# Performance work log

Measured on AMD Instinct MI355X. Metric: run time of the kernel, lower is better.

Reference implementation:

```python
import jax, jax.numpy as jnp
import numpy as np

N = 50000   # total nodes
E = 600000  # total edges
D = 128     # feature dim (node_dim == all gcn_dims)
G = 128     # graphs in batch
LN_EPS = 1e-5


def setup_inputs() -> dict:
    key = jax.random.key(0)
    ks = jax.random.split(key, 16)
    inp = {
        "x": jax.random.normal(ks[0], (N, D), dtype=jnp.float32),
        "edge_index": jax.random.randint(ks[1], (2, E), 0, N),
        "batch": jnp.sort(jax.random.randint(ks[2], (N,), 0, G)),
    }
    for l in range(3):
        inp[f"W{l}"] = jax.random.normal(ks[3 + 4 * l], (D, D), dtype=jnp.float32) / np.float32(np.sqrt(D))
        inp[f"b{l}"] = jnp.zeros((D,), jnp.float32)
        inp[f"g{l}"] = jnp.ones((D,), jnp.float32)   # LayerNorm weight
        inp[f"be{l}"] = jnp.zeros((D,), jnp.float32)  # LayerNorm bias
    return inp


def _gcn_norm(edge_index):
    # PyG GCNConv default: add self-loops, symmetric deg^-1/2 normalization.
    loop = jnp.arange(N, dtype=edge_index.dtype)
    src = jnp.concatenate([edge_index[0], loop])
    dst = jnp.concatenate([edge_index[1], loop])
    deg = jax.ops.segment_sum(jnp.ones(src.shape[0], jnp.float32), dst, num_segments=N)
    dinv = jnp.where(deg > 0, jax.lax.rsqrt(deg), 0.0)
    norm = dinv[src] * dinv[dst]  # [E+N]
    return src, dst, norm


def _block(x, src, dst, norm, W, b, g, be):
    # GCNConv: gather-transform-scatter
    h = x @ W                                   # [N, D]
    msg = h[src] * norm[:, None]                # [E+N, D] gather + scale
    out = jax.ops.segment_sum(msg, dst, num_segments=N) + b
    # LayerNorm
    mu = jnp.mean(out, axis=-1, keepdims=True)
    var = jnp.mean((out - mu) ** 2, axis=-1, keepdims=True)
    out = (out - mu) * jax.lax.rsqrt(var + LN_EPS) * g + be
    # residual (Identity since in==out channels) + SiLU
    return jax.nn.silu(out + x)


def reference(x, edge_index, batch, W0, b0, g0, be0, W1, b1, g1, be1, W2, b2, g2, be2):
    src, dst, norm = _gcn_norm(edge_index)
    params = [(W0, b0, g0, be0), (W1, b1, g1, be1), (W2, b2, g2, be2)]
    for (W, b, g, be) in params:
        x = _block(x, src, dst, norm, W, b, g, be)
    # global mean pool over batch ids
    counts = jax.ops.segment_sum(jnp.ones((N,), jnp.float32), batch, num_segments=G)
    sums = jax.ops.segment_sum(x, batch, num_segments=G)
    return sums / jnp.maximum(counts, 1.0)[:, None]
```

## Files before the change

kernel.cpp:

```cpp
#include <hip/hip_runtime.h>
#include <math.h>

#define DD 128

typedef __attribute__((ext_vector_type(8))) short short8;
typedef __attribute__((ext_vector_type(4))) float f32x4;

__device__ __forceinline__ unsigned short f2b(float f) {
    unsigned int x = __float_as_uint(f);
    return (unsigned short)((x + 0x7FFFu + ((x >> 16) & 1u)) >> 16);
}
__device__ __forceinline__ float b2f(unsigned short u) {
    return __uint_as_float(((unsigned int)u) << 16);
}

__global__ __launch_bounds__(256) void k_setup(const int* __restrict__ dst, int* __restrict__ cnt, int E,
                                               const float* __restrict__ W0, const float* __restrict__ W1,
                                               const float* __restrict__ W2, unsigned short* __restrict__ T0,
                                               unsigned short* __restrict__ T1, unsigned short* __restrict__ T2) {
    int bid = blockIdx.x;
    if (bid < 192) {
        int l = bid >> 6;
        const float* W = (l == 0) ? W0 : (l == 1) ? W1 : W2;
        unsigned short* WT = (l == 0) ? T0 : (l == 1) ? T1 : T2;
        int idx = (bid & 63) * 256 + threadIdx.x;
        int k = idx >> 7, c = idx & 127;
        WT[c * DD + k] = f2b(W[idx]);
    } else {
        int e = (bid - 192) * 256 + threadIdx.x;
        if (e < E) atomicAdd(&cnt[dst[e]], 1);
    }
}

__global__ __launch_bounds__(256) void k_scan1(const int* __restrict__ cnt, int* __restrict__ part, int N) {
    __shared__ int lds[256];
    int t = threadIdx.x;
    int i = blockIdx.x * 256 + t;
    lds[t] = (i < N) ? cnt[i] : 0;
    __syncthreads();
#pragma unroll
    for (int off = 128; off > 0; off >>= 1) {
        if (t < off) lds[t] += lds[t + off];
        __syncthreads();
    }
    if (t == 0) part[blockIdx.x] = lds[0];
}

__global__ __launch_bounds__(1024) void k_scan2(int* __restrict__ part, int* __restrict__ rowptr,
                                                int nblk, int N) {
    __shared__ int lds[1024];
    int t = threadIdx.x;
    int v = (t < nblk) ? part[t] : 0;
    lds[t] = v;
    __syncthreads();
    for (int off = 1; off < 1024; off <<= 1) {
        int u = (t >= off) ? lds[t - off] : 0;
        __syncthreads();
        lds[t] += u;
        __syncthreads();
    }
    if (t < nblk) part[t] = lds[t] - v;
    if (t == 1023) rowptr[N] = lds[1023];
}

__global__ __launch_bounds__(256) void k_scan3(const int* __restrict__ cnt, const int* __restrict__ part,
                                               int* __restrict__ rowptr, float* __restrict__ dinv, int N) {
    __shared__ int lds[256];
    int t = threadIdx.x;
    int i = blockIdx.x * 256 + t;
    int v = (i < N) ? cnt[i] : 0;
    lds[t] = v;
    __syncthreads();
    for (int off = 1; off < 256; off <<= 1) {
        int u = (t >= off) ? lds[t - off] : 0;
        __syncthreads();
        lds[t] += u;
        __syncthreads();
    }
    if (i < N) {
        rowptr[i] = part[blockIdx.x] + lds[t] - v;
        dinv[i] = rsqrtf((float)v + 1.0f);
    }
}

__global__ __launch_bounds__(256) void k_fill(const int* __restrict__ src, const int* __restrict__ dst,
                                              const float* __restrict__ dinv, const int* __restrict__ rowptr,
                                              int* __restrict__ cursor, int2* __restrict__ adj, int E) {
    int e = blockIdx.x * 256 + threadIdx.x;
    if (e >= E) return;
    int s = src[e], d = dst[e];
    int pos = atomicAdd(&cursor[d], 1);
    float w = dinv[s] * dinv[d];
    adj[rowptr[d] + pos] = make_int2(s, __float_as_int(w));
}

template <int IN_BF16>
__global__ __launch_bounds__(256) void k_gemm_mfma(const void* __restrict__ Xv,
                                                   const unsigned short* __restrict__ WT,
                                                   unsigned short* __restrict__ H, int N) {
    __shared__ __align__(16) unsigned short sB[DD * DD];
    __shared__ __align__(16) unsigned short sA[DD * DD];
    int tid = threadIdx.x;
    long row0 = (long)blockIdx.x * 128;

#pragma unroll
    for (int i = 0; i < 8; ++i) {
        int q = tid + 256 * i;
        int c = q >> 4, j = q & 15;
        short8 v = *(const short8*)(WT + q * 8);
        int byte = c * 256 + ((j * 16) ^ ((c & 7) << 4));
        *(short8*)((char*)sB + byte) = v;
    }
#pragma unroll
    for (int i = 0; i < 8; ++i) {
        int q = tid + 256 * i;
        int r = q >> 4, j = q & 15;
        short8 v;
        if (IN_BF16) {
#pragma unroll
            for (int z = 0; z < 8; ++z) v[z] = 0;
            if (row0 + r < N) v = *(const short8*)((const unsigned short*)Xv + (row0 + r) * DD + j * 8);
        } else {
            float4 a0 = make_float4(0.f, 0.f, 0.f, 0.f), a1 = a0;
            if (row0 + r < N) {
                const float4* p = (const float4*)((const float*)Xv + (row0 + r) * DD + j * 8);
                a0 = p[0];
                a1 = p[1];
            }
            v[0] = (short)f2b(a0.x); v[1] = (short)f2b(a0.y);
            v[2] = (short)f2b(a0.z); v[3] = (short)f2b(a0.w);
            v[4] = (short)f2b(a1.x); v[5] = (short)f2b(a1.y);
            v[6] = (short)f2b(a1.z); v[7] = (short)f2b(a1.w);
        }
        int byte = r * 256 + ((j * 16) ^ ((r & 7) << 4));
        *(short8*)((char*)sA + byte) = v;
    }
    __syncthreads();

    int w = tid >> 6, l = tid & 63;
    int lr = l & 15, kg = l >> 4;
    int ar0 = w * 32 + lr, ar1 = w * 32 + 16 + lr;
    f32x4 acc0[8] = {}, acc1[8] = {};

#pragma unroll
    for (int step = 0; step < 4; ++step) {
        int koff = step * 64 + kg * 16;
        short8 a0 = *(const short8*)((const char*)sA + ar0 * 256 + (koff ^ ((ar0 & 7) << 4)));
        short8 a1 = *(const short8*)((const char*)sA + ar1 * 256 + (koff ^ ((ar1 & 7) << 4)));
#pragma unroll
        for (int ct = 0; ct < 8; ++ct) {
            int c = ct * 16 + lr;
            short8 bf = *(const short8*)((const char*)sB + c * 256 + (koff ^ ((c & 7) << 4)));
            acc0[ct] = __builtin_amdgcn_mfma_f32_16x16x32_bf16(a0, bf, acc0[ct], 0, 0, 0);
            acc1[ct] = __builtin_amdgcn_mfma_f32_16x16x32_bf16(a1, bf, acc1[ct], 0, 0, 0);
        }
    }

#pragma unroll
    for (int ct = 0; ct < 8; ++ct) {
#pragma unroll
        for (int reg = 0; reg < 4; ++reg) {
            long r = row0 + w * 32 + kg * 4 + reg;
            if (r < N) H[r * DD + ct * 16 + lr] = f2b(acc0[ct][reg]);
            long r2 = r + 16;
            if (r2 < N) H[r2 * DD + ct * 16 + lr] = f2b(acc1[ct][reg]);
        }
    }
}

template <int IN_BF16>
__global__ __launch_bounds__(256) void k_agg(const unsigned short* __restrict__ h, const void* __restrict__ xin,
                                             const int* __restrict__ rowptr, const int2* __restrict__ adj,
                                             const float* __restrict__ dinv, const float* __restrict__ b,
                                             const float* __restrict__ g, const float* __restrict__ be,
                                             unsigned int* __restrict__ xout, int N) {
    int row = blockIdx.x * 4 + (threadIdx.x >> 6);
    if (row >= N) return;
    int lane = threadIdx.x & 63;
    const unsigned int* hu = (const unsigned int*)h;

    float dv = dinv[row];
    float dv2 = dv * dv;
    unsigned int us = hu[(size_t)row * 64 + lane];
    float2 bv = ((const float2*)b)[lane];
    float2 acc = make_float2(fmaf(b2f((unsigned short)(us & 0xFFFF)), dv2, bv.x),
                             fmaf(b2f((unsigned short)(us >> 16)), dv2, bv.y));

    int beg = rowptr[row], end = rowptr[row + 1];
    for (int j0 = beg; j0 < end; j0 += 64) {
        int myj = j0 + lane;
        int2 a = make_int2(0, 0);
        if (myj < end) a = adj[myj];
        int cnt = min(64, end - j0);
        int cntR = (cnt + 15) & ~15;
        for (int k0 = 0; k0 < cntR; k0 += 16) {
            unsigned int un[16];
            float wt[16];
#pragma unroll
            for (int u = 0; u < 16; ++u) {
                int s = __shfl(a.x, k0 + u, 64);
                wt[u] = __int_as_float(__shfl(a.y, k0 + u, 64));
                un[u] = hu[(size_t)s * 64 + lane];
            }
#pragma unroll
            for (int u = 0; u < 16; ++u) {
                acc.x = fmaf(wt[u], b2f((unsigned short)(un[u] & 0xFFFF)), acc.x);
                acc.y = fmaf(wt[u], b2f((unsigned short)(un[u] >> 16)), acc.y);
            }
        }
    }

    float ssum = acc.x + acc.y;
#pragma unroll
    for (int o = 32; o > 0; o >>= 1) ssum += __shfl_xor(ssum, o, 64);
    float mu = ssum * (1.0f / 128.0f);
    float dx0 = acc.x - mu, dx1 = acc.y - mu;
    float vs = dx0 * dx0 + dx1 * dx1;
#pragma unroll
    for (int o = 32; o > 0; o >>= 1) vs += __shfl_xor(vs, o, 64);
    float rstd = rsqrtf(vs * (1.0f / 128.0f) + 1e-5f);

    float2 gv = ((const float2*)g)[lane];
    float2 bev = ((const float2*)be)[lane];
    float2 xv;
    if (IN_BF16) {
        unsigned int xu = ((const unsigned int*)xin)[(size_t)row * 64 + lane];
        xv = make_float2(b2f((unsigned short)(xu & 0xFFFF)), b2f((unsigned short)(xu >> 16)));
    } else {
        xv = ((const float2*)xin)[(size_t)row * 64 + lane];
    }
    float a0 = fmaf(dx0 * rstd, gv.x, bev.x) + xv.x;
    float a1 = fmaf(dx1 * rstd, gv.y, bev.y) + xv.y;
    a0 = a0 / (1.0f + expf(-a0));
    a1 = a1 / (1.0f + expf(-a1));
    xout[(size_t)row * 64 + lane] = ((unsigned int)f2b(a1) << 16) | (unsigned int)f2b(a0);
}

__global__ __launch_bounds__(256) void k_pool2(const unsigned int* __restrict__ x, const int* __restrict__ batch,
                                               float* __restrict__ out, int N) {
    int gi = blockIdx.x;
    int lo = 0, hi = N;
    while (lo < hi) { int m = (lo + hi) >> 1; if (batch[m] < gi) lo = m + 1; else hi = m; }
    int beg = lo;
    lo = beg; hi = N;
    while (lo < hi) { int m = (lo + hi) >> 1; if (batch[m] < gi + 1) lo = m + 1; else hi = m; }
    int end = lo;

    int tid = threadIdx.x;
    int wave = tid >> 6, lane = tid & 63;
    float2 acc = make_float2(0.f, 0.f);
    for (int r = beg + wave; r < end; r += 4) {
        unsigned int u = x[(size_t)r * 64 + lane];
        acc.x += b2f((unsigned short)(u & 0xFFFF));
        acc.y += b2f((unsigned short)(u >> 16));
    }
    __shared__ float part[4][DD];
    ((float2*)part[wave])[lane] = acc;
    __syncthreads();
    if (wave == 0) {
        float sx = 0.f, sy = 0.f;
#pragma unroll
        for (int w = 0; w < 4; ++w) {
            float2 v = ((const float2*)part[w])[lane];
            sx += v.x;
            sy += v.y;
        }
        float inv = 1.0f / fmaxf((float)(end - beg), 1.0f);
        ((float2*)(out + (size_t)gi * DD))[lane] = make_float2(sx * inv, sy * inv);
    }
}

extern "C" void kernel_launch(void* const* d_in, const int* in_sizes, int n_in,
                              void* d_out, int out_size, void* d_ws, size_t ws_size,
                              hipStream_t stream) {
    const float* x = (const float*)d_in[0];
    const int* edge = (const int*)d_in[1];
    const int* batch = (const int*)d_in[2];
    const float* W[3] = {(const float*)d_in[3], (const float*)d_in[7], (const float*)d_in[11]};
    const float* b[3] = {(const float*)d_in[4], (const float*)d_in[8], (const float*)d_in[12]};
    const float* g[3] = {(const float*)d_in[5], (const float*)d_in[9], (const float*)d_in[13]};
    const float* be[3] = {(const float*)d_in[6], (const float*)d_in[10], (const float*)d_in[14]};

    int N = in_sizes[0] / DD;
    int E = in_sizes[1] / 2;
    int G = out_size / DD;
    const int* srcI = edge;
    const int* dstI = edge + E;

    int nblk = (N + 255) / 256;

    char* ws = (char*)d_ws;
    size_t ND = (size_t)N * DD;
    unsigned int* bufX = (unsigned int*)ws;           ws += ND * 2;
    unsigned short* bufH = (unsigned short*)ws;       ws += ND * 2;
    unsigned short* wt[3];
    for (int l = 0; l < 3; ++l) { wt[l] = (unsigned short*)ws; ws += (size_t)DD * DD * 2; }
    float* dinv = (float*)ws;                         ws += (size_t)N * 4;
    int* cnt = (int*)ws;                              ws += (size_t)N * 4;
    int* cursor = (int*)ws;                           ws += (size_t)N * 4;
    int* rowptr = (int*)ws;                           ws += (size_t)(N + 1) * 4;
    int* part = (int*)ws;                             ws += (size_t)nblk * 4;
    ws = (char*)(((uintptr_t)ws + 15) & ~(uintptr_t)15);
    int2* adj = (int2*)ws;

    hipMemsetAsync(cnt, 0, (size_t)N * 2 * 4, stream);

    k_setup<<<192 + (E + 255) / 256, 256, 0, stream>>>(dstI, cnt, E, W[0], W[1], W[2], wt[0], wt[1], wt[2]);
    k_scan1<<<nblk, 256, 0, stream>>>(cnt, part, N);
    k_scan2<<<1, 1024, 0, stream>>>(part, rowptr, nblk, N);
    k_scan3<<<nblk, 256, 0, stream>>>(cnt, part, rowptr, dinv, N);
    k_fill<<<(E + 255) / 256, 256, 0, stream>>>(srcI, dstI, dinv, rowptr, cursor, adj, E);

    int gblk = (N + 127) / 128, ablk = (N + 3) / 4;
    k_gemm_mfma<0><<<gblk, 256, 0, stream>>>(x, wt[0], bufH, N);
    k_agg<0><<<ablk, 256, 0, stream>>>(bufH, x, rowptr, adj, dinv, b[0], g[0], be[0], bufX, N);
    for (int l = 1; l < 3; ++l) {
        k_gemm_mfma<1><<<gblk, 256, 0, stream>>>(bufX, wt[l], bufH, N);
        k_agg<1><<<ablk, 256, 0, stream>>>(bufH, bufX, rowptr, adj, dinv, b[l], g[l], be[l], bufX, N);
    }

    k_pool2<<<G, 256, 0, stream>>>(bufX, batch, (float*)d_out, N);
}
```

Baseline: 238.8 us.

## Fold GCN normalization into GEMM output and bucket CSR build

The source-side deg^-1/2 scale now happens in the GEMM epilogue, and the destination-side scale is applied once after aggregation. This lets the adjacency store only 4-byte source indices instead of (src, weight) pairs, halving index traffic in each of the three aggregation passes. The CSR fill is split into a bucketed binning pass over 32-node buckets plus a per-bucket placement pass that uses LDS atomics, replacing global per-node atomics. The cost is an extra kernel and a temporary edge buffer, and rounding changes slightly because the scale is applied before the bf16 conversion.

```diff
diff --git a/kernel.cpp b/kernel.cpp
--- a/kernel.cpp
+++ b/kernel.cpp
@@ -83,20 +83,38 @@
     }
 }
 
-__global__ __launch_bounds__(256) void k_fill(const int* __restrict__ src, const int* __restrict__ dst,
-                                              const float* __restrict__ dinv, const int* __restrict__ rowptr,
-                                              int* __restrict__ cursor, int2* __restrict__ adj, int E) {
+__global__ __launch_bounds__(256) void k_bin(const int* __restrict__ src, const int* __restrict__ dst,
+                                             const int* __restrict__ rowptr, int* __restrict__ bcur,
+                                             int2* __restrict__ tmp, int E) {
     int e = blockIdx.x * 256 + threadIdx.x;
     if (e >= E) return;
     int s = src[e], d = dst[e];
-    int pos = atomicAdd(&cursor[d], 1);
-    float w = dinv[s] * dinv[d];
-    adj[rowptr[d] + pos] = make_int2(s, __float_as_int(w));
+    int b = d >> 5;
+    int base = rowptr[b << 5];
+    int slot = atomicAdd(&bcur[b], 1);
+    tmp[base + slot] = make_int2(s, d);
+}
+
+__global__ __launch_bounds__(256) void k_place(const int* __restrict__ rowptr, const int2* __restrict__ tmp,
+                                               int* __restrict__ adjS, int N) {
+    int b = blockIdx.x;
+    int d0 = b << 5;
+    int dend = min(d0 + 32, N);
+    int base = rowptr[d0], endp = rowptr[dend];
+    __shared__ int lcur[32];
+    if (threadIdx.x < 32) lcur[threadIdx.x] = 0;
+    __syncthreads();
+    for (int i = base + threadIdx.x; i < endp; i += 256) {
+        int2 sd = tmp[i];
+        int pos = atomicAdd(&lcur[sd.y - d0], 1);
+        adjS[rowptr[sd.y] + pos] = sd.x;
+    }
 }
 
 template <int IN_BF16>
 __global__ __launch_bounds__(256) void k_gemm_mfma(const void* __restrict__ Xv,
                                                    const unsigned short* __restrict__ WT,
+                                                   const float* __restrict__ dinv,
                                                    unsigned short* __restrict__ H, int N) {
     __shared__ __align__(16) unsigned short sB[DD * DD];
     __shared__ __align__(16) unsigned short sA[DD * DD];
@@ -156,21 +174,28 @@
         }
     }
 
+    float dv0[4], dv1[4];
+#pragma unroll
+    for (int reg = 0; reg < 4; ++reg) {
+        long r = row0 + w * 32 + kg * 4 + reg;
+        dv0[reg] = (r < N) ? dinv[r] : 0.f;
+        dv1[reg] = (r + 16 < N) ? dinv[r + 16] : 0.f;
+    }
 #pragma unroll
     for (int ct = 0; ct < 8; ++ct) {
 #pragma unroll
         for (int reg = 0; reg < 4; ++reg) {
             long r = row0 + w * 32 + kg * 4 + reg;
-            if (r < N) H[r * DD + ct * 16 + lr] = f2b(acc0[ct][reg]);
+            if (r < N) H[r * DD + ct * 16 + lr] = f2b(dv0[reg] * acc0[ct][reg]);
             long r2 = r + 16;
-            if (r2 < N) H[r2 * DD + ct * 16 + lr] = f2b(acc1[ct][reg]);
+            if (r2 < N) H[r2 * DD + ct * 16 + lr] = f2b(dv1[reg] * acc1[ct][reg]);
         }
     }
 }
 
 template <int IN_BF16>
 __global__ __launch_bounds__(256) void k_agg(const unsigned short* __restrict__ h, const void* __restrict__ xin,
-                                             const int* __restrict__ rowptr, const int2* __restrict__ adj,
+                                             const int* __restrict__ rowptr, const int* __restrict__ adjS,
                                              const float* __restrict__ dinv, const float* __restrict__ b,
                                              const float* __restrict__ g, const float* __restrict__ be,
                                              unsigned int* __restrict__ xout, int N) {
@@ -180,41 +205,42 @@
     const unsigned int* hu = (const unsigned int*)h;
 
     float dv = dinv[row];
-    float dv2 = dv * dv;
     unsigned int us = hu[(size_t)row * 64 + lane];
-    float2 bv = ((const float2*)b)[lane];
-    float2 acc = make_float2(fmaf(b2f((unsigned short)(us & 0xFFFF)), dv2, bv.x),
-                             fmaf(b2f((unsigned short)(us >> 16)), dv2, bv.y));
+    float selfx = b2f((unsigned short)(us & 0xFFFF));
+    float selfy = b2f((unsigned short)(us >> 16));
+    float2 acc = make_float2(0.f, 0.f);
 
     int beg = rowptr[row], end = rowptr[row + 1];
     for (int j0 = beg; j0 < end; j0 += 64) {
         int myj = j0 + lane;
-        int2 a = make_int2(0, 0);
-        if (myj < end) a = adj[myj];
+        int a = (myj < end) ? adjS[myj] : 0;
         int cnt = min(64, end - j0);
         int cntR = (cnt + 15) & ~15;
         for (int k0 = 0; k0 < cntR; k0 += 16) {
             unsigned int un[16];
-            float wt[16];
 #pragma unroll
             for (int u = 0; u < 16; ++u) {
-                int s = __shfl(a.x, k0 + u, 64);
-                wt[u] = __int_as_float(__shfl(a.y, k0 + u, 64));
+                int s = __shfl(a, k0 + u, 64);
                 un[u] = hu[(size_t)s * 64 + lane];
             }
 #pragma unroll
             for (int u = 0; u < 16; ++u) {
-                acc.x = fmaf(wt[u], b2f((unsigned short)(un[u] & 0xFFFF)), acc.x);
-                acc.y = fmaf(wt[u], b2f((unsigned short)(un[u] >> 16)), acc.y);
+                float m = (k0 + u < cnt) ? 1.0f : 0.0f;
+                acc.x = fmaf(m, b2f((unsigned short)(un[u] & 0xFFFF)), acc.x);
+                acc.y = fmaf(m, b2f((unsigned short)(un[u] >> 16)), acc.y);
             }
         }
     }
 
-    float ssum = acc.x + acc.y;
+    float2 bv = ((const float2*)b)[lane];
+    float ox = fmaf(dv, selfx + acc.x, bv.x);
+    float oy = fmaf(dv, selfy + acc.y, bv.y);
+
+    float ssum = ox + oy;
 #pragma unroll
     for (int o = 32; o > 0; o >>= 1) ssum += __shfl_xor(ssum, o, 64);
     float mu = ssum * (1.0f / 128.0f);
-    float dx0 = acc.x - mu, dx1 = acc.y - mu;
+    float dx0 = ox - mu, dx1 = oy - mu;
     float vs = dx0 * dx0 + dx1 * dx1;
 #pragma unroll
     for (int o = 32; o > 0; o >>= 1) vs += __shfl_xor(vs, o, 64);
@@ -288,6 +314,7 @@
     const int* dstI = edge + E;
 
     int nblk = (N + 255) / 256;
+    int nbuck = (N + 31) / 32;
 
     char* ws = (char*)d_ws;
     size_t ND = (size_t)N * DD;
@@ -297,26 +324,28 @@
     for (int l = 0; l < 3; ++l) { wt[l] = (unsigned short*)ws; ws += (size_t)DD * DD * 2; }
     float* dinv = (float*)ws;                         ws += (size_t)N * 4;
     int* cnt = (int*)ws;                              ws += (size_t)N * 4;
-    int* cursor = (int*)ws;                           ws += (size_t)N * 4;
+    int* bcur = (int*)ws;                             ws += (size_t)nbuck * 4;
     int* rowptr = (int*)ws;                           ws += (size_t)(N + 1) * 4;
     int* part = (int*)ws;                             ws += (size_t)nblk * 4;
     ws = (char*)(((uintptr_t)ws + 15) & ~(uintptr_t)15);
-    int2* adj = (int2*)ws;
-
-    hipMemsetAsync(cnt, 0, (size_t)N * 2 * 4, stream);
+    int2* tmp = (int2*)ws;                            ws += (size_t)E * 8;
+    int* adjS = (int*)ws;
+
+    hipMemsetAsync(cnt, 0, ((size_t)N + nbuck) * 4, stream);
 
     k_setup<<<192 + (E + 255) / 256, 256, 0, stream>>>(dstI, cnt, E, W[0], W[1], W[2], wt[0], wt[1], wt[2]);
     k_scan1<<<nblk, 256, 0, stream>>>(cnt, part, N);
     k_scan2<<<1, 1024, 0, stream>>>(part, rowptr, nblk, N);
     k_scan3<<<nblk, 256, 0, stream>>>(cnt, part, rowptr, dinv, N);
-    k_fill<<<(E + 255) / 256, 256, 0, stream>>>(srcI, dstI, dinv, rowptr, cursor, adj, E);
+    k_bin<<<(E + 255) / 256, 256, 0, stream>>>(srcI, dstI, rowptr, bcur, tmp, E);
+    k_place<<<nbuck, 256, 0, stream>>>(rowptr, tmp, adjS, N);
 
     int gblk = (N + 127) / 128, ablk = (N + 3) / 4;
-    k_gemm_mfma<0><<<gblk, 256, 0, stream>>>(x, wt[0], bufH, N);
-    k_agg<0><<<ablk, 256, 0, stream>>>(bufH, x, rowptr, adj, dinv, b[0], g[0], be[0], bufX, N);
+    k_gemm_mfma<0><<<gblk, 256, 0, stream>>>(x, wt[0], dinv, bufH, N);
+    k_agg<0><<<ablk, 256, 0, stream>>>(bufH, x, rowptr, adjS, dinv, b[0], g[0], be[0], bufX, N);
     for (int l = 1; l < 3; ++l) {
-        k_gemm_mfma<1><<<gblk, 256, 0, stream>>>(bufX, wt[l], bufH, N);
-        k_agg<1><<<ablk, 256, 0, stream>>>(bufH, bufX, rowptr, adj, dinv, b[l], g[l], be[l], bufX, N);
+        k_gemm_mfma<1><<<gblk, 256, 0, stream>>>(bufX, wt[l], dinv, bufH, N);
+        k_agg<1><<<ablk, 256, 0, stream>>>(bufH, bufX, rowptr, adjS, dinv, b[l], g[l], be[l], bufX, N);
     }
 
     k_pool2<<<G, 256, 0, stream>>>(bufX, batch, (float*)d_out, N);
```

Result: slower. 338.4 us (+41.7%).
